# Kernel optimization log

Measured on AMD Instinct MI355X. Metric: run time of the kernel, lower is better.

## Reference

```python
import jax, jax.numpy as jnp
import numpy as np

N, E, H, D, HD, L, G = 50000, 800000, 8, 16, 128, 6, 64
ND, ED, FF = 48, 4, 512


def _ln(x, g, b):
    m = x.mean(-1, keepdims=True)
    v = ((x - m) ** 2).mean(-1, keepdims=True)
    return (x - m) * jax.lax.rsqrt(v + 1e-5) * g + b


def setup_inputs() -> dict:
    key = jax.random.key(0)
    ks = iter(jax.random.split(key, 64))

    def rn(shape, s=0.05):
        return jax.random.normal(next(ks), shape, jnp.float32) * s

    inp = {
        "h": jax.random.normal(next(ks), (N, ND), jnp.float32),
        "e": jax.random.normal(next(ks), (E, ED), jnp.float32),
        "edge_index": jax.random.randint(next(ks), (2, E), 0, N),
        "batch": jnp.sort(jax.random.randint(next(ks), (N,), 0, G)),
        "node_W": rn((ND, HD)), "node_b": jnp.zeros(HD, jnp.float32),
        "edge_W": rn((ED, HD)), "edge_b": jnp.zeros(HD, jnp.float32),
        "Wq": rn((L, HD, HD)), "bq": jnp.zeros((L, HD), jnp.float32),
        "Wk": rn((L, HD, HD)), "bk": jnp.zeros((L, HD), jnp.float32),
        "Wv": rn((L, HD, HD)), "bv": jnp.zeros((L, HD), jnp.float32),
        "Wo": rn((L, HD, HD)), "bo": jnp.zeros((L, HD), jnp.float32),
        "Web": rn((L, HD, H)), "beb": jnp.zeros((L, H), jnp.float32),
        "W1": rn((L, HD, FF)), "b1": jnp.zeros((L, FF), jnp.float32),
        "W2": rn((L, FF, HD)), "b2": jnp.zeros((L, HD), jnp.float32),
        "g1": jnp.ones((L, HD), jnp.float32), "be1": jnp.zeros((L, HD), jnp.float32),
        "g2": jnp.ones((L, HD), jnp.float32), "be2": jnp.zeros((L, HD), jnp.float32),
        "gF": jnp.ones(HD, jnp.float32), "bF": jnp.zeros(HD, jnp.float32),
    }
    return inp


def reference(h, e, edge_index, batch, node_W, node_b, edge_W, edge_b,
              Wq, bq, Wk, bk, Wv, bv, Wo, bo, Web, beb,
              W1, b1, W2, b2, g1, be1, g2, be2, gF, bF):
    x = h @ node_W + node_b            # [N, HD]
    ee = e @ edge_W + edge_b           # [E, HD]
    row, col = edge_index[0], edge_index[1]
    n = x.shape[0]
    scale = 1.0 / np.sqrt(D).astype(np.float32)
    for l in range(L):
        res = x
        xn = _ln(x, g1[l], be1[l])
        q = (xn @ Wq[l] + bq[l]).reshape(n, H, D)
        k = (xn @ Wk[l] + bk[l]).reshape(n, H, D)
        v = (xn @ Wv[l] + bv[l]).reshape(n, H, D)
        # per-edge scores [E, H] with edge bias
        s = (q[row] * k[col]).sum(-1) * scale + (ee @ Web[l] + beb[l])
        # segment softmax over incoming edges of each row node
        mx = jax.ops.segment_max(s, row, num_segments=n)
        ex = jnp.exp(s - mx[row])
        den = jax.ops.segment_sum(ex, row, num_segments=n)[row] + 1e-10
        p = ex / den                   # [E, H]
        out = jax.ops.segment_sum(p[..., None] * v[col], row, num_segments=n)
        x = out.reshape(n, HD) @ Wo[l] + bo[l] + res
        res = x
        xn = _ln(x, g2[l], be2[l])
        x = jax.nn.relu(xn @ W1[l] + b1[l]) @ W2[l] + b2[l] + res
    x = _ln(x, gF, bF)
    cnt = jax.ops.segment_sum(jnp.ones((n,), x.dtype), batch, num_segments=G)
    gsum = jax.ops.segment_sum(x, batch, num_segments=G)
    graph_emb = gsum / jnp.maximum(cnt, 1.0)[:, None]
    return x, graph_emb
```

## Files before the change

### kernel.cpp

```cpp
#include <hip/hip_runtime.h>
#include <hip/hip_bf16.h>
#include <math.h>

#define NN 50000
#define EE 800000
#define HH 8
#define DD 16
#define HDIM 128
#define LL 6
#define GG 64
#define NDI 48
#define EDI 4
#define FFD 512
#define SCB ((NN + 1023) / 1024)

typedef __attribute__((ext_vector_type(8))) short short8;
typedef __attribute__((ext_vector_type(8))) unsigned short ushort8;
typedef __attribute__((ext_vector_type(4))) float floatx4;
typedef __attribute__((ext_vector_type(2))) float f32x2;

__device__ __forceinline__ unsigned short f2bf(float f) {
  unsigned u = __builtin_bit_cast(unsigned, f);
  unsigned rnd = 0x7FFFu + ((u >> 16) & 1u);
  return (unsigned short)((u + rnd) >> 16);
}
__device__ __forceinline__ float bf2f(unsigned short u) {
  unsigned v = ((unsigned)u) << 16;
  return __builtin_bit_cast(float, v);
}

#ifdef __has_builtin
#if __has_builtin(__builtin_amdgcn_cvt_pk_f32_fp8) && __has_builtin(__builtin_amdgcn_cvt_pk_fp8_f32)
#define HW_FP8 1
#endif
#endif

__device__ __forceinline__ unsigned char f2fp8(float f) {
#ifdef HW_FP8
  int p = __builtin_amdgcn_cvt_pk_fp8_f32(f, 0.f, 0, false);
  return (unsigned char)(p & 0xff);
#else
  unsigned u = __builtin_bit_cast(unsigned, f);
  unsigned s = (u >> 24) & 0x80u;
  unsigned au = u & 0x7fffffffu;
  float a = __builtin_bit_cast(float, au);
  if (a >= 448.f) return (unsigned char)(s | 0x7e);
  if (a < 0.0009765625f) return (unsigned char)s;
  int e32 = (int)(au >> 23) - 127;
  if (e32 >= -6) {
    au += (1u << 19);
    e32 = (int)(au >> 23) - 127;
    if (e32 > 8) return (unsigned char)(s | 0x7e);
    unsigned m = (au >> 20) & 7u;
    return (unsigned char)(s | (unsigned)((e32 + 7) << 3) | m);
  } else {
    int m = (int)(a * 512.f + 0.5f);
    if (m > 7) return (unsigned char)(s | 0x08);
    return (unsigned char)(s | (unsigned)m);
  }
#endif
}

__device__ __forceinline__ void fp8x8_dec(uint2 kw, float* f) {
#ifdef HW_FP8
  f32x2 a = __builtin_amdgcn_cvt_pk_f32_fp8((int)kw.x, false);
  f32x2 b = __builtin_amdgcn_cvt_pk_f32_fp8((int)kw.x, true);
  f32x2 c = __builtin_amdgcn_cvt_pk_f32_fp8((int)kw.y, false);
  f32x2 d = __builtin_amdgcn_cvt_pk_f32_fp8((int)kw.y, true);
  f[0] = a[0]; f[1] = a[1]; f[2] = b[0]; f[3] = b[1];
  f[4] = c[0]; f[5] = c[1]; f[6] = d[0]; f[7] = d[1];
#else
  unsigned w[2] = {kw.x, kw.y};
#pragma unroll
  for (int i = 0; i < 8; i++) {
    unsigned char bb = (unsigned char)((w[i >> 2] >> ((i & 3) * 8)) & 0xff);
    unsigned s = ((unsigned)bb & 0x80u) << 24;
    unsigned e = (bb >> 3) & 0xFu;
    unsigned m = bb & 7u;
    float v;
    if (e == 0) v = (float)m * 0.001953125f;
    else v = __builtin_bit_cast(float, ((e + 120u) << 23) | (m << 20));
    f[i] = __builtin_bit_cast(float, __builtin_bit_cast(unsigned, v) | s);
  }
#endif
}

__global__ void k_node_proj(const float* __restrict__ h, const float* __restrict__ W,
                            const float* __restrict__ b, float* __restrict__ x) {
  __shared__ float hs[32][NDI];
  int t = threadIdx.x;
  int n0 = blockIdx.x * 32;
  for (int idx = t; idx < 32 * NDI; idx += 128) {
    int nb = idx / NDI, i = idx - nb * NDI;
    int node = n0 + nb;
    hs[nb][i] = (node < NN) ? h[node * NDI + i] : 0.f;
  }
  __syncthreads();
  float acc[32];
#pragma unroll
  for (int nb = 0; nb < 32; nb++) acc[nb] = 0.f;
  for (int i = 0; i < NDI; i++) {
    float w = W[i * HDIM + t];
#pragma unroll
    for (int nb = 0; nb < 32; nb++) acc[nb] += hs[nb][i] * w;
  }
  float bb = b[t];
  for (int nb = 0; nb < 32; nb++) {
    int node = n0 + nb;
    if (node < NN) x[node * HDIM + t] = acc[nb] + bb;
  }
}

__global__ void k_pack(const float* __restrict__ W, unsigned short* __restrict__ dst,
                       int K, int OC, int nmat) {
  int KC = K >> 5, CT = OC >> 4;
  int total = nmat * CT * KC * 512;
  for (int i = blockIdx.x * 256 + threadIdx.x; i < total; i += gridDim.x * 256) {
    int j = i & 7;
    int lane = (i >> 3) & 63;
    int rest = i >> 9;
    int kc = rest % KC; rest /= KC;
    int ct = rest % CT; int m = rest / CT;
    int col = ct * 16 + (lane & 15);
    int k = kc * 32 + (lane >> 4) * 8 + j;
    dst[i] = f2bf(W[(size_t)m * K * OC + (size_t)k * OC + col]);
  }
}

__global__ void k_wcomb(const float* __restrict__ edge_W, const float* __restrict__ edge_b,
                        const float* __restrict__ Web, const float* __restrict__ beb,
                        float* __restrict__ Wcomb, float* __restrict__ bcomb) {
  int t = threadIdx.x;
  if (t < LL * EDI * HH) {
    int l = t / (EDI * HH);
    int i = (t / HH) % EDI;
    int hh = t % HH;
    float s = 0.f;
    for (int j = 0; j < HDIM; j++) s += edge_W[i * HDIM + j] * Web[(l * HDIM + j) * HH + hh];
    Wcomb[t] = s;
  } else if (t < LL * EDI * HH + LL * HH) {
    int u = t - LL * EDI * HH;
    int l = u / HH, hh = u % HH;
    float s = beb[l * HH + hh];
    for (int j = 0; j < HDIM; j++) s += edge_b[j] * Web[(l * HDIM + j) * HH + hh];
    bcomb[u] = s;
  }
}

__global__ void k_deg(const int* __restrict__ row, int* __restrict__ deg) {
  int e = blockIdx.x * 256 + threadIdx.x;
  if (e < EE) atomicAdd(&deg[row[e]], 1);
}

__global__ void k_scan1(const int* __restrict__ deg, int* __restrict__ bsum) {
  __shared__ int red[256];
  int b = blockIdx.x, t = threadIdx.x;
  int base = b * 1024;
  int s = 0;
  for (int j = t; j < 1024; j += 256) {
    int i = base + j;
    s += (i < NN) ? deg[i] : 0;
  }
  red[t] = s;
  __syncthreads();
  for (int off = 128; off > 0; off >>= 1) {
    if (t < off) red[t] += red[t + off];
    __syncthreads();
  }
  if (t == 0) bsum[b] = red[0];
}

__global__ void k_scan2(int* __restrict__ bsum, int* __restrict__ starts) {
  if (threadIdx.x == 0) {
    int s = 0;
    for (int b = 0; b < SCB; b++) { int v = bsum[b]; bsum[b] = s; s += v; }
    starts[NN] = s;
  }
}

__global__ void k_scan3(const int* __restrict__ deg, const int* __restrict__ bsum,
                        int* __restrict__ starts, int* __restrict__ cursor) {
  __shared__ int tsum[256];
  int b = blockIdx.x, t = threadIdx.x;
  int base = b * 1024 + t * 4;
  int v[4];
  int s = 0;
#pragma unroll
  for (int j = 0; j < 4; j++) {
    int i = base + j;
    v[j] = (i < NN) ? deg[i] : 0;
    s += v[j];
  }
  tsum[t] = s;
  __syncthreads();
  for (int off = 1; off < 256; off <<= 1) {
    int xv = (t >= off) ? tsum[t - off] : 0;
    __syncthreads();
    tsum[t] += xv;
    __syncthreads();
  }
  int excl = tsum[t] - s + bsum[b];
#pragma unroll
  for (int j = 0; j < 4; j++) {
    int i = base + j;
    if (i < NN) { starts[i] = excl; cursor[i] = excl; excl += v[j]; }
  }
}

__global__ void k_scatter(const int* __restrict__ row, const int* __restrict__ col,
                          int* __restrict__ cursor,
                          int* __restrict__ eids, int* __restrict__ cols) {
  int e = blockIdx.x * 256 + threadIdx.x;
  if (e < EE) {
    int r = row[e];
    int pos = atomicAdd(&cursor[r], 1);
    eids[pos] = e;
    cols[pos] = col[e];
  }
}

__global__ void k_gbounds(const int* __restrict__ batch, int* __restrict__ gstart) {
  int i = blockIdx.x * 256 + threadIdx.x;
  if (i >= NN) return;
  int b = batch[i];
  int prev = (i == 0) ? -1 : batch[i - 1];
  for (int g = prev + 1; g <= b; g++) gstart[g] = i;
  if (i == NN - 1) {
    for (int g = b + 1; g <= GG; g++) gstart[g] = NN;
  }
}

__global__ void k_ebias(const int* __restrict__ eids, const float* __restrict__ efeat,
                        const float* __restrict__ Wcomb, const float* __restrict__ bcomb,
                        float* __restrict__ ebias) {
  int i = blockIdx.x * 256 + threadIdx.x;
  if (i >= EE) return;
  int e = eids[i];
  float4 ef = *(const float4*)(efeat + (size_t)e * EDI);
  float o[8];
#pragma unroll
  for (int hh = 0; hh < HH; hh++) {
    o[hh] = bcomb[hh] + ef.x * Wcomb[hh] + ef.y * Wcomb[8 + hh] +
            ef.z * Wcomb[16 + hh] + ef.w * Wcomb[24 + hh];
  }
  float4 o0 = {o[0], o[1], o[2], o[3]};
  float4 o1 = {o[4], o[5], o[6], o[7]};
  *(float4*)(ebias + (size_t)i * 8) = o0;
  *(float4*)(ebias + (size_t)i * 8 + 4) = o1;
}

__global__ __launch_bounds__(256) void k_ln_qkv_mfma(
    const float* __restrict__ x,
    const unsigned short* __restrict__ Wqf, const float* __restrict__ bq,
    const unsigned short* __restrict__ Wkf, const float* __restrict__ bk,
    const unsigned short* __restrict__ Wvf, const float* __restrict__ bv,
    const float* __restrict__ g, const float* __restrict__ be,
    unsigned short* __restrict__ q, unsigned char* __restrict__ kf8,
    unsigned short* __restrict__ v) {
  __shared__ unsigned short xn[64][136];
  int t = threadIdx.x;
  int n0 = blockIdx.x * 64;
  {
    int row = t >> 2, quad = t & 3;
    int node = n0 + row;
    float xv[32];
    float s = 0.f, sq = 0.f;
    if (node < NN) {
      const float* xr = x + (size_t)node * HDIM + quad * 32;
#pragma unroll
      for (int c = 0; c < 8; c++) {
        float4 f = *(const float4*)(xr + c * 4);
        xv[c*4+0]=f.x; xv[c*4+1]=f.y; xv[c*4+2]=f.z; xv[c*4+3]=f.w;
      }
#pragma unroll
      for (int j = 0; j < 32; j++) { s += xv[j]; sq += xv[j]*xv[j]; }
    } else {
#pragma unroll
      for (int j = 0; j < 32; j++) xv[j] = 0.f;
    }
    s += __shfl_xor(s, 1); s += __shfl_xor(s, 2);
    sq += __shfl_xor(sq, 1); sq += __shfl_xor(sq, 2);
    float m = s * (1.f / HDIM);
    float rv = rsqrtf(sq * (1.f / HDIM) - m * m + 1e-5f);
#pragma unroll
    for (int cb = 0; cb < 4; cb++) {
      ushort8 u;
#pragma unroll
      for (int j = 0; j < 8; j++) {
        int col = quad * 32 + cb * 8 + j;
        u[j] = f2bf((xv[cb*8+j] - m) * rv * g[col] + be[col]);
      }
      *(ushort8*)&xn[row][quad * 32 + cb * 8] = u;
    }
  }
  __syncthreads();
  int w = t >> 6, lane = t & 63;
  int r0 = w * 16;
  short8 a[4];
#pragma unroll
  for (int kc = 0; kc < 4; kc++)
    a[kc] = *(const short8*)&xn[r0 + (lane & 15)][kc * 32 + (lane >> 4) * 8];
  const unsigned short* Wf[3] = {Wqf, Wkf, Wvf};
  const float* bias[3] = {bq, bk, bv};
#pragma unroll
  for (int mm = 0; mm < 3; mm++) {
    const unsigned short* wf = Wf[mm];
    for (int ct = 0; ct < 8; ct++) {
      floatx4 acc = {0.f, 0.f, 0.f, 0.f};
#pragma unroll
      for (int kc = 0; kc < 4; kc++) {
        short8 b = *(const short8*)(wf + ((size_t)(ct * 4 + kc) * 64 + lane) * 8);
        acc = __builtin_amdgcn_mfma_f32_16x16x32_bf16(a[kc], b, acc, 0, 0, 0);
      }
      int col = ct * 16 + (lane & 15);
      float bb = bias[mm][col];
#pragma unroll
      for (int r = 0; r < 4; r++) {
        int rr = r0 + (lane >> 4) * 4 + r;
        int nd = n0 + rr;
        if (nd < NN) {
          float val = acc[r] + bb;
          if (mm == 0) q[(size_t)nd * HDIM + col] = f2bf(val);
          else if (mm == 1) kf8[(size_t)nd * HDIM + col] = f2fp8(val);
          else v[(size_t)nd * HDIM + col] = f2bf(val);
        }
      }
    }
  }
}

__global__ __launch_bounds__(256) void k_attn(
    const unsigned short* __restrict__ q, const unsigned char* __restrict__ kf8,
    const unsigned short* __restrict__ v,
    const int* __restrict__ cols, const float* __restrict__ ebias,
    const int* __restrict__ starts,
    unsigned short* __restrict__ out) {
  int t = threadIdx.x;
  int wave = t >> 6, lane = t & 63;
  int g = lane >> 4, d = lane & 15;
  int node = blockIdx.x * 16 + wave * 4 + g;
  if (node >= NN) return;
  int hh = d >> 1;

  float qf[8];
  {
    ushort8 q8 = *(const ushort8*)(q + (size_t)node * HDIM + d * 8);
#pragma unroll
    for (int j = 0; j < 8; j++) qf[j] = bf2f(q8[j]) * 0.25f;
  }

  int s0 = starts[node], s1 = starts[node + 1];
  float acc[8];
#pragma unroll
  for (int j = 0; j < 8; j++) acc[j] = 0.f;
  float lsum = 0.f;

  uint2 sk[4];
  ushort8 sv[4];
  float seb[4];
  int pc[4];
  float peb[4];

#pragma unroll
  for (int j = 0; j < 4; j++) {
    int i = s0 + j;
    bool ok = i < s1;
    int c = ok ? cols[i] : 0;
    sk[j] = *(const uint2*)(kf8 + (size_t)c * HDIM + d * 8);
    sv[j] = *(const ushort8*)(v + (size_t)c * HDIM + d * 8);
    seb[j] = ok ? ebias[(size_t)i * 8 + hh] : -1e30f;
  }
#pragma unroll
  for (int j = 0; j < 4; j++) {
    int i = s0 + 4 + j;
    bool ok = i < s1;
    pc[j] = ok ? cols[i] : 0;
    peb[j] = ok ? ebias[(size_t)i * 8 + hh] : -1e30f;
  }

  for (int base = s0; base < s1; base += 4) {
#pragma unroll
    for (int j = 0; j < 4; j++) {
      int c = pc[j];
      uint2 kn = *(const uint2*)(kf8 + (size_t)c * HDIM + d * 8);
      ushort8 vn = *(const ushort8*)(v + (size_t)c * HDIM + d * 8);
      float ebn = peb[j];
      int i2 = base + 8 + j;
      bool ok2 = i2 < s1;
      int c2 = ok2 ? cols[i2] : 0;
      float eb2 = ok2 ? ebias[(size_t)i2 * 8 + hh] : -1e30f;
      float kf[8];
      fp8x8_dec(sk[j], kf);
      float part = 0.f;
#pragma unroll
      for (int u = 0; u < 8; u++) part += qf[u] * kf[u];
      part += __shfl_xor(part, 1);
      float ex = __expf(part + seb[j]);
      lsum += ex;
#pragma unroll
      for (int u = 0; u < 8; u++) acc[u] += ex * bf2f(sv[j][u]);
      sk[j] = kn; sv[j] = vn; seb[j] = ebn;
      pc[j] = c2; peb[j] = eb2;
    }
  }

  float inv = 1.f / (lsum + 1e-10f);
  ushort8 o;
#pragma unroll
  for (int j = 0; j < 8; j++) o[j] = f2bf(acc[j] * inv);
  *(ushort8*)(out + (size_t)node * HDIM + d * 8) = o;
}

__global__ __launch_bounds__(256) void k_oproj_ffn(
    const unsigned short* __restrict__ ao, const unsigned short* __restrict__ Wof,
    const float* __restrict__ bo,
    const unsigned short* __restrict__ W1f, const float* __restrict__ b1,
    const unsigned short* __restrict__ W2f, const float* __restrict__ b2,
    const float* __restrict__ g, const float* __restrict__ be,
    float* __restrict__ x) {
  __shared__ unsigned short hs[32][520];
  __shared__ float xr[32][132];
  __shared__ unsigned short xn[32][136];
  unsigned short* aosp = &hs[0][0];
  int t = threadIdx.x;
  int n0 = blockIdx.x * 32;

#pragma unroll
  for (int c = 0; c < 2; c++) {
    int elem = c * 2048 + t * 8;
    int row = elem >> 7, col = elem & 127;
    int nd = n0 + row;
    ushort8 u = {0, 0, 0, 0, 0, 0, 0, 0};
    if (nd < NN) u = *(const ushort8*)(ao + (size_t)nd * HDIM + col);
    *(ushort8*)&aosp[row * 136 + col] = u;
  }
#pragma unroll
  for (int c = 0; c < 4; c++) {
    int elem = c * 1024 + t * 4;
    int row = elem >> 7, col = elem & 127;
    int nd = n0 + row;
    float4 f = {0.f, 0.f, 0.f, 0.f};
    if (nd < NN) f = *(const float4*)(x + (size_t)nd * HDIM + col);
    *(float4*)&xr[row][col] = f;
  }
  __syncthreads();

  int w = t >> 6, lane = t & 63;
  int rt = w & 1, r0 = rt * 16;
  int cthalf = w >> 1;

  {
    short8 a[4];
#pragma unroll
    for (int kc = 0; kc < 4; kc++)
      a[kc] = *(const short8*)&aosp[(r0 + (lane & 15)) * 136 + kc * 32 + (lane >> 4) * 8];
#pragma unroll
    for (int ci = 0; ci < 4; ci++) {
      int ct = cthalf * 4 + ci;
      floatx4 acc = {0.f, 0.f, 0.f, 0.f};
#pragma unroll
      for (int kc = 0; kc < 4; kc++) {
        short8 b = *(const short8*)(Wof + ((size_t)(ct * 4 + kc) * 64 + lane) * 8);
        acc = __builtin_amdgcn_mfma_f32_16x16x32_bf16(a[kc], b, acc, 0, 0, 0);
      }
      int col = ct * 16 + (lane & 15);
      float bb = bo[col];
#pragma unroll
      for (int r = 0; r < 4; r++) {
        int rr = r0 + (lane >> 4) * 4 + r;
        xr[rr][col] += acc[r] + bb;
      }
    }
  }
  __syncthreads();

  {
    int row = t >> 3, oct = t & 7;
    float xv[16];
    float s = 0.f, sq = 0.f;
#pragma unroll
    for (int jj = 0; jj < 16; jj++) {
      float f = xr[row][oct * 16 + jj];
      xv[jj] = f; s += f; sq += f * f;
    }
    s += __shfl_xor(s, 1); s += __shfl_xor(s, 2); s += __shfl_xor(s, 4);
    sq += __shfl_xor(sq, 1); sq += __shfl_xor(sq, 2); sq += __shfl_xor(sq, 4);
    float m = s * (1.f / HDIM);
    float rv = rsqrtf(sq * (1.f / HDIM) - m * m + 1e-5f);
#pragma unroll
    for (int cb = 0; cb < 2; cb++) {
      ushort8 u;
#pragma unroll
      for (int jj = 0; jj < 8; jj++) {
        int col = oct * 16 + cb * 8 + jj;
        u[jj] = f2bf((xv[cb*8+jj] - m) * rv * g[col] + be[col]);
      }
      *(ushort8*)&xn[row][oct * 16 + cb * 8] = u;
    }
  }
  __syncthreads();

  {
    short8 a[4];
#pragma unroll
    for (int kc = 0; kc < 4; kc++)
      a[kc] = *(const short8*)&xn[r0 + (lane & 15)][kc * 32 + (lane >> 4) * 8];
    for (int ci = 0; ci < 16; ci++) {
      int ct = cthalf * 16 + ci;
      floatx4 acc = {0.f, 0.f, 0.f, 0.f};
#pragma unroll
      for (int kc = 0; kc < 4; kc++) {
        short8 b = *(const short8*)(W1f + ((size_t)(ct * 4 + kc) * 64 + lane) * 8);
        acc = __builtin_amdgcn_mfma_f32_16x16x32_bf16(a[kc], b, acc, 0, 0, 0);
      }
      int col = ct * 16 + (lane & 15);
      float bb = b1[col];
#pragma unroll
      for (int r = 0; r < 4; r++) {
        int rr = r0 + (lane >> 4) * 4 + r;
        hs[rr][col] = f2bf(fmaxf(acc[r] + bb, 0.f));
      }
    }
  }
  __syncthreads();

  {
    short8 ah[16];
#pragma unroll
    for (int kc = 0; kc < 16; kc++)
      ah[kc] = *(const short8*)&hs[r0 + (lane & 15)][kc * 32 + (lane >> 4) * 8];
#pragma unroll
    for (int ci = 0; ci < 4; ci++) {
      int ct = cthalf * 4 + ci;
      floatx4 acc = {0.f, 0.f, 0.f, 0.f};
#pragma unroll
      for (int kc = 0; kc < 16; kc++) {
        short8 b = *(const short8*)(W2f + ((size_t)(ct * 16 + kc) * 64 + lane) * 8);
        acc = __builtin_amdgcn_mfma_f32_16x16x32_bf16(ah[kc], b, acc, 0, 0, 0);
      }
      int col = ct * 16 + (lane & 15);
      float bb = b2[col];
#pragma unroll
      for (int r = 0; r < 4; r++) {
        int rr = r0 + (lane >> 4) * 4 + r;
        int nd = n0 + rr;
        if (nd < NN) x[(size_t)nd * HDIM + col] = xr[rr][col] + acc[r] + bb;
      }
    }
  }
}

__global__ __launch_bounds__(256) void k_final(
    const float* __restrict__ x, const float* __restrict__ g,
    const float* __restrict__ be, float* __restrict__ outx) {
  int t = threadIdx.x;
  int row = t >> 2, quad = t & 3;
  int node = blockIdx.x * 64 + row;
  if (node >= NN) return;
  const float* xr = x + (size_t)node * HDIM + quad * 32;
  float xv[32];
  float s = 0.f, sq = 0.f;
#pragma unroll
  for (int c = 0; c < 8; c++) {
    float4 f = *(const float4*)(xr + c * 4);
    xv[c*4+0]=f.x; xv[c*4+1]=f.y; xv[c*4+2]=f.z; xv[c*4+3]=f.w;
  }
#pragma unroll
  for (int j = 0; j < 32; j++) { s += xv[j]; sq += xv[j]*xv[j]; }
  s += __shfl_xor(s, 1); s += __shfl_xor(s, 2);
  sq += __shfl_xor(sq, 1); sq += __shfl_xor(sq, 2);
  float m = s * (1.f / HDIM);
  float rv = rsqrtf(sq * (1.f / HDIM) - m * m + 1e-5f);
  float* orow = outx + (size_t)node * HDIM + quad * 32;
#pragma unroll
  for (int c = 0; c < 8; c++) {
    float4 o;
    int col = quad * 32 + c * 4;
    o.x = (xv[c*4+0] - m) * rv * g[col+0] + be[col+0];
    o.y = (xv[c*4+1] - m) * rv * g[col+1] + be[col+1];
    o.z = (xv[c*4+2] - m) * rv * g[col+2] + be[col+2];
    o.w = (xv[c*4+3] - m) * rv * g[col+3] + be[col+3];
    *(float4*)(orow + c * 4) = o;
  }
}

__global__ void k_pool(const float* __restrict__ outx, const int* __restrict__ gstart,
                       float* __restrict__ outg) {
  __shared__ float part[4][HDIM];
  int g = blockIdx.x;
  int t = threadIdx.x;
  int hd = t & 127, p = t >> 7;
  int s0 = gstart[g];
  int c = gstart[g + 1] - s0;
  float s = 0.f;
  for (int i = p; i < c; i += 4) s += outx[(size_t)(s0 + i) * HDIM + hd];
  part[p][hd] = s;
  __syncthreads();
  if (p == 0) {
    float tot = part[0][hd] + part[1][hd] + part[2][hd] + part[3][hd];
    outg[g * HDIM + hd] = tot / fmaxf((float)c, 1.f);
  }
}

extern "C" void kernel_launch(void* const* d_in, const int* in_sizes, int n_in,
                              void* d_out, int out_size, void* d_ws, size_t ws_size,
                              hipStream_t stream) {
  const float* h      = (const float*)d_in[0];
  const float* e      = (const float*)d_in[1];
  const int*   eidx   = (const int*)d_in[2];
  const int*   batch  = (const int*)d_in[3];
  const float* node_W = (const float*)d_in[4];
  const float* node_b = (const float*)d_in[5];
  const float* edge_W = (const float*)d_in[6];
  const float* edge_b = (const float*)d_in[7];
  const float* Wq  = (const float*)d_in[8];
  const float* bq  = (const float*)d_in[9];
  const float* Wk  = (const float*)d_in[10];
  const float* bk  = (const float*)d_in[11];
  const float* Wv  = (const float*)d_in[12];
  const float* bv  = (const float*)d_in[13];
  const float* Wo  = (const float*)d_in[14];
  const float* bo  = (const float*)d_in[15];
  const float* Web = (const float*)d_in[16];
  const float* beb = (const float*)d_in[17];
  const float* W1  = (const float*)d_in[18];
  const float* b1  = (const float*)d_in[19];
  const float* W2  = (const float*)d_in[20];
  const float* b2  = (const float*)d_in[21];
  const float* g1  = (const float*)d_in[22];
  const float* be1 = (const float*)d_in[23];
  const float* g2  = (const float*)d_in[24];
  const float* be2 = (const float*)d_in[25];
  const float* gF  = (const float*)d_in[26];
  const float* bF  = (const float*)d_in[27];

  const int* rowArr = eidx;
  const int* colArr = eidx + EE;

  char* ws = (char*)d_ws;
  size_t off = 0;
  auto alloc = [&](size_t bytes) -> void* {
    void* p = ws + off;
    off = (off + bytes + 255) & ~(size_t)255;
    return p;
  };
  float* x    = (float*)alloc((size_t)NN * HDIM * 4);
  unsigned short* qb  = (unsigned short*)alloc((size_t)NN * HDIM * 2);
  unsigned char*  kf8 = (unsigned char*)alloc((size_t)NN * HDIM);
  unsigned short* vb  = (unsigned short*)alloc((size_t)NN * HDIM * 2);
  unsigned short* ao  = (unsigned short*)alloc((size_t)NN * HDIM * 2);
  int* deg    = (int*)alloc((size_t)NN * 4);
  int* starts = (int*)alloc((size_t)(NN + 1) * 4);
  int* cursor = (int*)alloc((size_t)NN * 4);
  int* eids   = (int*)alloc((size_t)EE * 4);
  int* cols   = (int*)alloc((size_t)EE * 4);
  float* ebias = (float*)alloc((size_t)EE * HH * 4);
  int* bsum   = (int*)alloc((size_t)SCB * 4);
  float* Wcomb = (float*)alloc((size_t)LL * EDI * HH * 4);
  float* bcomb = (float*)alloc((size_t)LL * HH * 4);
  int* gstart = (int*)alloc((size_t)(GG + 1) * 4);
  const int QKV_FRAG = 8 * 4 * 512;
  const int FFN_FRAG1 = 32 * 4 * 512;
  const int FFN_FRAG2 = 8 * 16 * 512;
  unsigned short* Wqf = (unsigned short*)alloc((size_t)LL * QKV_FRAG * 2);
  unsigned short* Wkf = (unsigned short*)alloc((size_t)LL * QKV_FRAG * 2);
  unsigned short* Wvf = (unsigned short*)alloc((size_t)LL * QKV_FRAG * 2);
  unsigned short* Wof = (unsigned short*)alloc((size_t)LL * QKV_FRAG * 2);
  unsigned short* W1f = (unsigned short*)alloc((size_t)LL * FFN_FRAG1 * 2);
  unsigned short* W2f = (unsigned short*)alloc((size_t)LL * FFN_FRAG2 * 2);

  hipMemsetAsync(deg, 0, (size_t)NN * 4, stream);

  k_node_proj<<<(NN + 31) / 32, 128, 0, stream>>>(h, node_W, node_b, x);
  k_wcomb<<<1, 256, 0, stream>>>(edge_W, edge_b, Web, beb, Wcomb, bcomb);
  k_pack<<<(LL * QKV_FRAG + 255) / 256, 256, 0, stream>>>(Wq, Wqf, HDIM, HDIM, LL);
  k_pack<<<(LL * QKV_FRAG + 255) / 256, 256, 0, stream>>>(Wk, Wkf, HDIM, HDIM, LL);
  k_pack<<<(LL * QKV_FRAG + 255) / 256, 256, 0, stream>>>(Wv, Wvf, HDIM, HDIM, LL);
  k_pack<<<(LL * QKV_FRAG + 255) / 256, 256, 0, stream>>>(Wo, Wof, HDIM, HDIM, LL);
  k_pack<<<(LL * FFN_FRAG1 + 255) / 256, 256, 0, stream>>>(W1, W1f, HDIM, FFD, LL);
  k_pack<<<(LL * FFN_FRAG2 + 255) / 256, 256, 0, stream>>>(W2, W2f, FFD, HDIM, LL);
  k_deg<<<(EE + 255) / 256, 256, 0, stream>>>(rowArr, deg);
  k_scan1<<<SCB, 256, 0, stream>>>(deg, bsum);
  k_scan2<<<1, 64, 0, stream>>>(bsum, starts);
  k_scan3<<<SCB, 256, 0, stream>>>(deg, bsum, starts, cursor);
  k_scatter<<<(EE + 255) / 256, 256, 0, stream>>>(rowArr, colArr, cursor, eids, cols);
  k_gbounds<<<(NN + 255) / 256, 256, 0, stream>>>(batch, gstart);

  int nb64 = (NN + 63) / 64;
  int nb32 = (NN + 31) / 32;
  int nb16 = (NN + 15) / 16;
  int nbE  = (EE + 255) / 256;
  for (int l = 0; l < LL; l++) {
    k_ln_qkv_mfma<<<nb64, 256, 0, stream>>>(x,
        Wqf + (size_t)l * QKV_FRAG, bq + (size_t)l * HDIM,
        Wkf + (size_t)l * QKV_FRAG, bk + (size_t)l * HDIM,
        Wvf + (size_t)l * QKV_FRAG, bv + (size_t)l * HDIM,
        g1 + (size_t)l * HDIM, be1 + (size_t)l * HDIM, qb, kf8, vb);
    k_ebias<<<nbE, 256, 0, stream>>>(eids, e,
        Wcomb + (size_t)l * EDI * HH, bcomb + (size_t)l * HH, ebias);
    k_attn<<<nb16, 256, 0, stream>>>(qb, kf8, vb, cols, ebias, starts, ao);
    k_oproj_ffn<<<nb32, 256, 0, stream>>>(ao, Wof + (size_t)l * QKV_FRAG,
        bo + (size_t)l * HDIM,
        W1f + (size_t)l * FFN_FRAG1, b1 + (size_t)l * FFD,
        W2f + (size_t)l * FFN_FRAG2, b2 + (size_t)l * HDIM,
        g2 + (size_t)l * HDIM, be2 + (size_t)l * HDIM, x);
  }

  float* outx = (float*)d_out;
  float* outg = outx + (size_t)NN * HDIM;
  k_final<<<(NN + 63) / 64, 256, 0, stream>>>(x, gF, bF, outx);
  k_pool<<<GG, 512, 0, stream>>>(outx, gstart, outg);
}
```

Before: 1.233 ms.

## Shrink LDS in fused o-proj/FFN kernel by keeping residual in registers and chunking FF

The fused output-projection + FFN kernel no longer stages the fp32 residual tile in shared memory. The residual is read straight from global into registers, and LayerNorm row statistics are reduced with shuffles plus a small cross-wave LDS buffer. The 512-wide FFN hidden layer is processed in two 256-column passes that accumulate the second GEMM in registers, halving the hidden buffer. The goal is to cut LDS use per block so more blocks fit per CU, at the cost of extra barriers, more live registers, and uncoalesced residual loads.

Result: slower. 1.441 ms (+16.8%).

```diff
diff --git a/kernel.cpp b/kernel.cpp
--- a/kernel.cpp
+++ b/kernel.cpp
@@ -418,9 +418,9 @@
     const unsigned short* __restrict__ W2f, const float* __restrict__ b2,
     const float* __restrict__ g, const float* __restrict__ be,
     float* __restrict__ x) {
-  __shared__ unsigned short hs[32][520];
-  __shared__ float xr[32][132];
+  __shared__ unsigned short hs[32][264];
   __shared__ unsigned short xn[32][136];
+  __shared__ float red[2][32][2];
   unsigned short* aosp = &hs[0][0];
   int t = threadIdx.x;
   int n0 = blockIdx.x * 32;
@@ -434,26 +434,19 @@
     if (nd < NN) u = *(const ushort8*)(ao + (size_t)nd * HDIM + col);
     *(ushort8*)&aosp[row * 136 + col] = u;
   }
-#pragma unroll
-  for (int c = 0; c < 4; c++) {
-    int elem = c * 1024 + t * 4;
-    int row = elem >> 7, col = elem & 127;
-    int nd = n0 + row;
-    float4 f = {0.f, 0.f, 0.f, 0.f};
-    if (nd < NN) f = *(const float4*)(x + (size_t)nd * HDIM + col);
-    *(float4*)&xr[row][col] = f;
-  }
   __syncthreads();
 
   int w = t >> 6, lane = t & 63;
   int rt = w & 1, r0 = rt * 16;
   int cthalf = w >> 1;
-
+  int lcol = lane & 15, lrow4 = (lane >> 4) * 4;
+
+  float racc[4][4];
   {
     short8 a[4];
 #pragma unroll
     for (int kc = 0; kc < 4; kc++)
-      a[kc] = *(const short8*)&aosp[(r0 + (lane & 15)) * 136 + kc * 32 + (lane >> 4) * 8];
+      a[kc] = *(const short8*)&aosp[(r0 + lcol) * 136 + kc * 32 + (lane >> 4) * 8];
 #pragma unroll
     for (int ci = 0; ci < 4; ci++) {
       int ct = cthalf * 4 + ci;
@@ -463,89 +456,120 @@
         short8 b = *(const short8*)(Wof + ((size_t)(ct * 4 + kc) * 64 + lane) * 8);
         acc = __builtin_amdgcn_mfma_f32_16x16x32_bf16(a[kc], b, acc, 0, 0, 0);
       }
-      int col = ct * 16 + (lane & 15);
+      int col = ct * 16 + lcol;
       float bb = bo[col];
 #pragma unroll
       for (int r = 0; r < 4; r++) {
-        int rr = r0 + (lane >> 4) * 4 + r;
-        xr[rr][col] += acc[r] + bb;
+        int nd = n0 + r0 + lrow4 + r;
+        float res = (nd < NN) ? x[(size_t)nd * HDIM + col] : 0.f;
+        racc[ci][r] = res + acc[r] + bb;
+      }
+    }
+  }
+
+  {
+    float ps[4], pq[4];
+#pragma unroll
+    for (int r = 0; r < 4; r++) { ps[r] = 0.f; pq[r] = 0.f; }
+#pragma unroll
+    for (int ci = 0; ci < 4; ci++)
+#pragma unroll
+      for (int r = 0; r < 4; r++) {
+        float f = racc[ci][r];
+        ps[r] += f; pq[r] += f * f;
+      }
+#pragma unroll
+    for (int r = 0; r < 4; r++) {
+      ps[r] += __shfl_xor(ps[r], 1); pq[r] += __shfl_xor(pq[r], 1);
+      ps[r] += __shfl_xor(ps[r], 2); pq[r] += __shfl_xor(pq[r], 2);
+      ps[r] += __shfl_xor(ps[r], 4); pq[r] += __shfl_xor(pq[r], 4);
+      ps[r] += __shfl_xor(ps[r], 8); pq[r] += __shfl_xor(pq[r], 8);
+      if (lcol == 0) {
+        int rr = r0 + lrow4 + r;
+        red[cthalf][rr][0] = ps[r];
+        red[cthalf][rr][1] = pq[r];
       }
     }
   }
   __syncthreads();
 
   {
-    int row = t >> 3, oct = t & 7;
-    float xv[16];
-    float s = 0.f, sq = 0.f;
-#pragma unroll
-    for (int jj = 0; jj < 16; jj++) {
-      float f = xr[row][oct * 16 + jj];
-      xv[jj] = f; s += f; sq += f * f;
-    }
-    s += __shfl_xor(s, 1); s += __shfl_xor(s, 2); s += __shfl_xor(s, 4);
-    sq += __shfl_xor(sq, 1); sq += __shfl_xor(sq, 2); sq += __shfl_xor(sq, 4);
-    float m = s * (1.f / HDIM);
-    float rv = rsqrtf(sq * (1.f / HDIM) - m * m + 1e-5f);
-#pragma unroll
-    for (int cb = 0; cb < 2; cb++) {
-      ushort8 u;
-#pragma unroll
-      for (int jj = 0; jj < 8; jj++) {
-        int col = oct * 16 + cb * 8 + jj;
-        u[jj] = f2bf((xv[cb*8+jj] - m) * rv * g[col] + be[col]);
-      }
-      *(ushort8*)&xn[row][oct * 16 + cb * 8] = u;
+#pragma unroll
+    for (int r = 0; r < 4; r++) {
+      int rr = r0 + lrow4 + r;
+      float s = red[0][rr][0] + red[1][rr][0];
+      float sq = red[0][rr][1] + red[1][rr][1];
+      float m = s * (1.f / HDIM);
+      float rv = rsqrtf(sq * (1.f / HDIM) - m * m + 1e-5f);
+#pragma unroll
+      for (int ci = 0; ci < 4; ci++) {
+        int col = (cthalf * 4 + ci) * 16 + lcol;
+        xn[rr][col] = f2bf((racc[ci][r] - m) * rv * g[col] + be[col]);
+      }
     }
   }
   __syncthreads();
 
-  {
-    short8 a[4];
-#pragma unroll
-    for (int kc = 0; kc < 4; kc++)
-      a[kc] = *(const short8*)&xn[r0 + (lane & 15)][kc * 32 + (lane >> 4) * 8];
-    for (int ci = 0; ci < 16; ci++) {
-      int ct = cthalf * 16 + ci;
+  float c2acc[4][4];
+#pragma unroll
+  for (int ci = 0; ci < 4; ci++)
+#pragma unroll
+    for (int r = 0; r < 4; r++) c2acc[ci][r] = 0.f;
+
+  short8 axn[4];
+#pragma unroll
+  for (int kc = 0; kc < 4; kc++)
+    axn[kc] = *(const short8*)&xn[r0 + lcol][kc * 32 + (lane >> 4) * 8];
+
+#pragma unroll
+  for (int pass = 0; pass < 2; pass++) {
+    for (int ci = 0; ci < 8; ci++) {
+      int ct = pass * 16 + cthalf * 8 + ci;
       floatx4 acc = {0.f, 0.f, 0.f, 0.f};
 #pragma unroll
       for (int kc = 0; kc < 4; kc++) {
         short8 b = *(const short8*)(W1f + ((size_t)(ct * 4 + kc) * 64 + lane) * 8);
-        acc = __builtin_amdgcn_mfma_f32_16x16x32_bf16(a[kc], b, acc, 0, 0, 0);
-      }
-      int col = ct * 16 + (lane & 15);
-      float bb = b1[col];
+        acc = __builtin_amdgcn_mfma_f32_16x16x32_bf16(axn[kc], b, acc, 0, 0, 0);
+      }
+      int gcol = ct * 16 + lcol;
+      int lcol2 = gcol - pass * 256;
+      float bb = b1[gcol];
 #pragma unroll
       for (int r = 0; r < 4; r++) {
-        int rr = r0 + (lane >> 4) * 4 + r;
-        hs[rr][col] = f2bf(fmaxf(acc[r] + bb, 0.f));
-      }
-    }
-  }
-  __syncthreads();
-
-  {
-    short8 ah[16];
-#pragma unroll
-    for (int kc = 0; kc < 16; kc++)
-      ah[kc] = *(const short8*)&hs[r0 + (lane & 15)][kc * 32 + (lane >> 4) * 8];
-#pragma unroll
-    for (int ci = 0; ci < 4; ci++) {
-      int ct = cthalf * 4 + ci;
-      floatx4 acc = {0.f, 0.f, 0.f, 0.f};
-#pragma unroll
-      for (int kc = 0; kc < 16; kc++) {
-        short8 b = *(const short8*)(W2f + ((size_t)(ct * 16 + kc) * 64 + lane) * 8);
-        acc = __builtin_amdgcn_mfma_f32_16x16x32_bf16(ah[kc], b, acc, 0, 0, 0);
-      }
-      int col = ct * 16 + (lane & 15);
-      float bb = b2[col];
-#pragma unroll
-      for (int r = 0; r < 4; r++) {
-        int rr = r0 + (lane >> 4) * 4 + r;
-        int nd = n0 + rr;
-        if (nd < NN) x[(size_t)nd * HDIM + col] = xr[rr][col] + acc[r] + bb;
-      }
+        hs[r0 + lrow4 + r][lcol2] = f2bf(fmaxf(acc[r] + bb, 0.f));
+      }
+    }
+    __syncthreads();
+    {
+      short8 ah[8];
+#pragma unroll
+      for (int kc = 0; kc < 8; kc++)
+        ah[kc] = *(const short8*)&hs[r0 + lcol][kc * 32 + (lane >> 4) * 8];
+#pragma unroll
+      for (int ci = 0; ci < 4; ci++) {
+        int ct2 = cthalf * 4 + ci;
+        floatx4 acc = {0.f, 0.f, 0.f, 0.f};
+#pragma unroll
+        for (int kc = 0; kc < 8; kc++) {
+          int kcg = pass * 8 + kc;
+          short8 b = *(const short8*)(W2f + ((size_t)(ct2 * 16 + kcg) * 64 + lane) * 8);
+          acc = __builtin_amdgcn_mfma_f32_16x16x32_bf16(ah[kc], b, acc, 0, 0, 0);
+        }
+#pragma unroll
+        for (int r = 0; r < 4; r++) c2acc[ci][r] += acc[r];
+      }
+    }
+    if (pass == 0) __syncthreads();
+  }
+
+#pragma unroll
+  for (int ci = 0; ci < 4; ci++) {
+    int col = (cthalf * 4 + ci) * 16 + lcol;
+    float bb = b2[col];
+#pragma unroll
+    for (int r = 0; r < 4; r++) {
+      int nd = n0 + r0 + lrow4 + r;
+      if (nd < NN) x[(size_t)nd * HDIM + col] = racc[ci][r] + c2acc[ci][r] + bb;
     }
   }
 }
```
